# Performance work log

Measured on AMD Instinct MI355X. Metric: run time of the kernel, lower is better.

## Reference

```python
import jax, jax.numpy as jnp
import numpy as np

B, N, C, F, OUT = 4, 512, 1024, 1024, 1024
LOC = 128  # min(128, out_channels)
EPS_BN = 1e-5


def _batchnorm(x, g, b):
    # BatchNorm1d in training mode: biased batch stats over rows
    m = jnp.mean(x, axis=0)
    v = jnp.var(x, axis=0)
    return (x - m) / jnp.sqrt(v + EPS_BN) * g + b


def _relative_pe(loc):
    # loc: [N,4] (x,y,w,h) -> [N,N,LOC]; faithfully replicates the torch
    # cat([N,4N]) -> view(-1,4) interleaving of the original code.
    cx = loc[:, 0] + 0.5 * loc[:, 2]
    cy = loc[:, 1] + 0.5 * loc[:, 3]
    w, h = loc[:, 2], loc[:, 3]
    eps = jnp.float32(1e-3)
    dx = jnp.maximum(jnp.abs(cx[:, None] - cx[None, :]) / w[None, :], eps)
    dy = jnp.maximum(jnp.abs(cy[:, None] - cy[None, :]) / h[None, :], eps)
    dw = w[:, None] / w[None, :]
    dh = h[:, None] / h[None, :]
    delta = jnp.log(jnp.concatenate([dx, dy, dw, dh], axis=-1))  # [N,4N]
    delta = delta.reshape(-1, 4)                                  # [N*N,4]
    d = LOC // 8
    pe = jnp.exp(2.0 * jnp.arange(d, dtype=jnp.float32) / d * np.log(1000.0))
    ang = delta[:, :, None] / pe                                  # [N*N,4,d]
    emb = jnp.concatenate([jnp.sin(ang), jnp.cos(ang)], axis=-1)  # [N*N,4,2d]
    return emb.reshape(N, N, LOC)


def reference(box_features, boxes, bn1_g, bn1_b, Wq, bq, Wk, bk, Wv, bv, Wr, br, bn2_g, bn2_b):
    feat = _batchnorm(box_features, bn1_g, bn1_b).reshape(B, N, C)

    def per_image(f, loc):
        rel = jnp.squeeze(_relative_pe(loc) @ Wr + br, axis=-1)   # [N,N]
        q = f @ Wq + bq
        k = f @ Wk + bk
        v = f @ Wv + bv
        att = q @ k.T / jnp.sqrt(jnp.float32(F)) + jax.nn.log_softmax(rel, axis=-1)
        return jax.nn.softmax(att, axis=-1) @ v                   # [N,OUT]

    out = jax.vmap(per_image)(feat, boxes).reshape(B * N, OUT)
    return _batchnorm(out, bn2_g, bn2_b)


def setup_inputs() -> dict:
    key = jax.random.key(0)
    ks = jax.random.split(key, 10)
    box_features = jax.random.normal(ks[0], (B * N, C), dtype=jnp.float32)
    u = jax.random.uniform(ks[1], (B, N, 4), dtype=jnp.float32)
    xy = u[..., :2] * 800.0
    wh = 16.0 + u[..., 2:] * 240.0
    boxes = jnp.concatenate([xy, wh], axis=-1)
    s = 0.02
    return {
        "box_features": box_features,
        "boxes": boxes,
        "bn1_g": jnp.ones((C,), jnp.float32),
        "bn1_b": jnp.zeros((C,), jnp.float32),
        "Wq": jax.random.normal(ks[2], (C, F), jnp.float32) * s,
        "bq": jnp.zeros((F,), jnp.float32),
        "Wk": jax.random.normal(ks[3], (C, F), jnp.float32) * s,
        "bk": jnp.zeros((F,), jnp.float32),
        "Wv": jax.random.normal(ks[4], (C, OUT), jnp.float32) * s,
        "bv": jnp.zeros((OUT,), jnp.float32),
        "Wr": jax.random.normal(ks[5], (LOC, 1), jnp.float32) * s,
        "br": jnp.zeros((1,), jnp.float32),
        "bn2_g": jnp.ones((OUT,), jnp.float32),
        "bn2_b": jnp.zeros((OUT,), jnp.float32),
    }
```

## Files before the change

kernel.cpp:

```cpp
#include <hip/hip_runtime.h>
#include <math.h>

typedef __bf16 bf16;
typedef __attribute__((ext_vector_type(8))) __bf16 bf16x8;
typedef __attribute__((ext_vector_type(4))) __bf16 bf16x4;
typedef __attribute__((ext_vector_type(4))) float f32x4;

#define NCH1 128
#define RPC1 16

#define XD0   (-6.93f)
#define XSPAN (11.03f)
#define XINVH (1023.f / 11.03f)

__global__ __launch_bounds__(256)
void prep(const float* __restrict__ Wq, const float* __restrict__ Wk, const float* __restrict__ Wv,
          bf16* __restrict__ T0, bf16* __restrict__ T1, bf16* __restrict__ T2,
          const float* __restrict__ bq, const float* __restrict__ bk, float* __restrict__ biasqk,
          const float* __restrict__ X, float* __restrict__ psum, float* __restrict__ psq,
          const float* __restrict__ boxes, const float* __restrict__ Wr, const float* __restrict__ br,
          float* __restrict__ ent, float* __restrict__ tabs)
{
    __shared__ float tile[64][65];
    const int bid = blockIdx.x;
    const int tid = threadIdx.x;

    if (bid < 768) {
        const int mat = bid >> 8, g2 = bid & 255;
        const float* W = (mat == 0) ? Wq : (mat == 1) ? Wk : Wv;
        bf16* T        = (mat == 0) ? T0 : (mat == 1) ? T1 : T2;
        const int bx = (g2 & 15) * 64, by = (g2 >> 4) * 64;
        const int tx = tid & 63, ty = tid >> 6;
#pragma unroll
        for (int i = 0; i < 16; ++i)
            tile[ty + i * 4][tx] = W[(long)(by + ty + i * 4) * 1024 + bx + tx];
        __syncthreads();
#pragma unroll
        for (int i = 0; i < 16; ++i)
            T[(long)(bx + ty + i * 4) * 1024 + by + tx] = (bf16)tile[tx][ty + i * 4];
    } else if (bid < 896) {
        const int c4 = tid;
        const long r0 = (long)(bid - 768) * RPC1;
        const float4* Xv = (const float4*)X;
        float4 s = {0.f,0.f,0.f,0.f}, q = {0.f,0.f,0.f,0.f};
#pragma unroll
        for (int r = 0; r < RPC1; ++r) {
            float4 x = Xv[(r0 + r) * 256 + c4];
            s.x += x.x; s.y += x.y; s.z += x.z; s.w += x.w;
            q.x += x.x*x.x; q.y += x.y*x.y; q.z += x.z*x.z; q.w += x.w*x.w;
        }
        ((float4*)psum)[(bid - 768) * 256 + c4] = s;
        ((float4*)psq) [(bid - 768) * 256 + c4] = q;
    } else if (bid == 896) {
        for (int e = tid; e < 2048; e += 256) {
            float4 b4 = ((const float4*)boxes)[e];
            float w = b4.z, h = b4.w;
            ent[0*2048+e] = b4.x + 0.5f * w;
            ent[1*2048+e] = b4.y + 0.5f * h;
            ent[2*2048+e] = __logf(w);
            ent[3*2048+e] = __logf(h);
            ent[4*2048+e] = 1e-3f * w;
            ent[5*2048+e] = 1e-3f * h;
        }
        for (int i = tid; i < 2048; i += 256)
            biasqk[i] = (i < 1024) ? bq[i] : bk[i - 1024];
    } else {
        const int c = bid - 897;
        float* tb = tabs + c * 1024;
        const float brq = 0.25f * br[0];
        const float hstep = XSPAN / 1023.f;
        for (int e = tid; e < 1024; e += 256) {
            float d = XD0 + hstep * (float)e;
            float a = brq;
#pragma unroll
            for (int k = 0; k < 16; ++k) {
                float tk = exp2f(-1.24572303558f * (float)k);
                float s_, c_;
                __sincosf(d * tk, &s_, &c_);
                a += s_ * Wr[c * 32 + k] + c_ * Wr[c * 32 + 16 + k];
            }
            tb[e] = a;
        }
    }
}

template <int NCH_, int BF16OUT>
__global__ __launch_bounds__(256)
void bn_final_apply(const float* __restrict__ X, const float* __restrict__ psum,
                    const float* __restrict__ psq, const float* __restrict__ g,
                    const float* __restrict__ b, void* __restrict__ Yp)
{
    __shared__ float ls[4][64], lq[4][64], ssc[64], ssh[64];
    const int t  = threadIdx.x;
    const int cs = blockIdx.x;
    const int rc = blockIdx.y;
    const int col_l = t & 63, part = t >> 6;
    const int col = cs * 64 + col_l;
    constexpr int CPT = NCH_ / 4;
    float s = 0.f, q = 0.f;
#pragma unroll
    for (int i = 0; i < CPT; ++i) {
        int ch = part * CPT + i;
        s += psum[ch * 1024 + col];
        q += psq [ch * 1024 + col];
    }
    ls[part][col_l] = s; lq[part][col_l] = q;
    __syncthreads();
    if (t < 64) {
        float S = ls[0][t]+ls[1][t]+ls[2][t]+ls[3][t];
        float Q = lq[0][t]+lq[1][t]+lq[2][t]+lq[3][t];
        float m = S / 2048.f;
        float v = Q / 2048.f - m*m;
        float inv = 1.0f / sqrtf(v + 1e-5f);
        float sc = g[cs*64+t] * inv;
        ssc[t] = sc; ssh[t] = b[cs*64+t] - m*sc;
    }
    __syncthreads();
    const int f = t & 15, rsub = t >> 4;
    float4 sc4 = ((const float4*)ssc)[f];
    float4 sh4 = ((const float4*)ssh)[f];
#pragma unroll
    for (int it = 0; it < 8; ++it) {
        int row = rc*128 + it*16 + rsub;
        float4 x = ((const float4*)(X + (long)row*1024 + cs*64))[f];
        float4 rv;
        rv.x = x.x*sc4.x + sh4.x;
        rv.y = x.y*sc4.y + sh4.y;
        rv.z = x.z*sc4.z + sh4.z;
        rv.w = x.w*sc4.w + sh4.w;
        if constexpr (BF16OUT) {
            bf16x4 y;
            y[0]=(bf16)rv.x; y[1]=(bf16)rv.y; y[2]=(bf16)rv.z; y[3]=(bf16)rv.w;
            ((bf16x4*)((bf16*)Yp + (long)row*1024 + cs*64))[f] = y;
        } else {
            ((float4*)((float*)Yp + (long)row*1024 + cs*64))[f] = rv;
        }
    }
}

__device__ __forceinline__ float look(const float* tab, float d)
{
    float t = (d - XD0) * XINVH;
    t = fminf(fmaxf(t, 0.f), 1022.999f);
    float fi = floorf(t);
    int i = (int)fi;
    float a = tab[i], b = tab[i + 1];
    return a + (b - a) * (t - fi);
}

__device__ __forceinline__ void stage_tile_128x32(const bf16* __restrict__ src_base, int ld,
                                                  int row0, int k0, bf16* lds_base, int w, int l)
{
#pragma unroll
    for (int t = 0; t < 2; ++t) {
        int rchunk = w * 32 + t * 16;
        const bf16* src = src_base + (long)(row0 + rchunk + (l >> 2)) * ld + k0 + (l & 3) * 8;
        __builtin_amdgcn_global_load_lds((__attribute__((address_space(1))) void*)src,
                                         (__attribute__((address_space(3))) void*)(lds_base + rchunk * 32),
                                         16, 0, 0);
    }
}

__device__ __forceinline__ void stage64(const bf16* __restrict__ src_base, int ld,
                                        int row0, int k0, bf16* lds_base, int w, int l)
{
    const bf16* src = src_base + (long)(row0 + w * 16 + (l >> 2)) * ld + k0 + (l & 3) * 8;
    __builtin_amdgcn_global_load_lds((__attribute__((address_space(1))) void*)src,
                                     (__attribute__((address_space(3))) void*)(lds_base + w * 16 * 32),
                                     16, 0, 0);
}

template <int MODE>
__device__ __forceinline__ void gemm_body(
    const bf16* __restrict__ Ab, int lda, const bf16* __restrict__ Bb, int ldb,
    bf16* __restrict__ Cp, int ldc, int K, int bm, int bn,
    const float* __restrict__ bias, char* smem)
{
    bf16* As0 = (bf16*)smem;
    bf16* Bs0 = (bf16*)(smem + 16384);
    const int tid = threadIdx.x;
    const int w = tid >> 6, l = tid & 63;
    const int wr = w >> 1, wc = w & 1;

    f32x4 acc[4][4];
#pragma unroll
    for (int i = 0; i < 4; ++i)
#pragma unroll
        for (int j = 0; j < 4; ++j) acc[i][j] = (f32x4){0.f,0.f,0.f,0.f};

    const int nkt = K >> 5;
    stage_tile_128x32(Ab, lda, bm, 0, As0, w, l);
    stage_tile_128x32(Bb, ldb, bn, 0, Bs0, w, l);
    __syncthreads();

    const int fr = l & 15;
    const int ko = (l >> 4) * 8;

    for (int kt = 0; kt < nkt; ++kt) {
        const int cur = kt & 1;
        bf16* Asc = As0 + cur * 4096;
        bf16* Bsc = Bs0 + cur * 4096;
        if (kt + 1 < nkt) {
            stage_tile_128x32(Ab, lda, bm, (kt + 1) << 5, As0 + (cur ^ 1) * 4096, w, l);
            stage_tile_128x32(Bb, ldb, bn, (kt + 1) << 5, Bs0 + (cur ^ 1) * 4096, w, l);
        }
        bf16x8 af[4], bfv[4];
#pragma unroll
        for (int mi = 0; mi < 4; ++mi)
            af[mi] = *(const bf16x8*)(&Asc[(wr * 64 + mi * 16 + fr) * 32 + ko]);
#pragma unroll
        for (int ni = 0; ni < 4; ++ni)
            bfv[ni] = *(const bf16x8*)(&Bsc[(wc * 64 + ni * 16 + fr) * 32 + ko]);
#pragma unroll
        for (int mi = 0; mi < 4; ++mi)
#pragma unroll
            for (int ni = 0; ni < 4; ++ni)
                acc[mi][ni] = __builtin_amdgcn_mfma_f32_16x16x32_bf16(af[mi], bfv[ni], acc[mi][ni], 0, 0, 0);
        __syncthreads();
    }

    const int crow0 = bm + wr * 64 + (l >> 4) * 4;
    const int ccol0 = bn + wc * 64 + fr;
#pragma unroll
    for (int mi = 0; mi < 4; ++mi)
#pragma unroll
        for (int ni = 0; ni < 4; ++ni)
#pragma unroll
            for (int r = 0; r < 4; ++r) {
                const int row = crow0 + mi * 16 + r;
                const int col = ccol0 + ni * 16;
                const float v = acc[mi][ni][r];
                if constexpr (MODE == 0) {
                    Cp[(long)row * ldc + col] = (bf16)(v + bias[col]);
                } else {
                    Cp[(long)row * ldc + col] = (bf16)(v + bias[row]);
                }
            }
}

__global__ __launch_bounds__(256, 2)
void megaGEMM(const bf16* __restrict__ featbf, const bf16* __restrict__ WqkT,
              const bf16* __restrict__ WvT, bf16* __restrict__ qkbf, bf16* __restrict__ vTbf,
              const float* __restrict__ biasqk, const float* __restrict__ bv)
{
    __shared__ char smem[32768];
    const unsigned bid = (blockIdx.x % 8u) * 48u + (blockIdx.x / 8u);
    const unsigned g = bid / 3u, r = bid % 3u;
    if (r < 2) {
        const unsigned t = g * 2 + r;
        gemm_body<0>(featbf, 1024, WqkT, 1024, qkbf, 2048, 1024,
                     (t & 15) * 128, (t >> 4) * 128, biasqk, smem);
    } else {
        const int img = g >> 5, rem = g & 31;
        gemm_body<1>(WvT, 1024, featbf + (long)img * 524288, 1024,
                     vTbf + (long)img * 524288, 512, 1024,
                     (rem >> 2) * 128, (rem & 3) * 128, bv, smem);
    }
}

__global__ __launch_bounds__(256, 4)
void attn64(const bf16* __restrict__ qk, float* __restrict__ S0, float* __restrict__ S1,
            const float* __restrict__ ent, const float* __restrict__ tabs)
{
    __shared__ char smem[20480];
    const int img = blockIdx.z >> 1, kh = blockIdx.z & 1;
    const int bm = blockIdx.x * 64, bn = blockIdx.y * 64;
    const bf16* A = qk + (long)img * 1048576 + kh * 512;
    const bf16* B = qk + 1024 + (long)img * 1048576 + kh * 512;
    bf16* As0 = (bf16*)smem;
    bf16* Bs0 = (bf16*)(smem + 8192);

    const int tid = threadIdx.x;
    const int w = tid >> 6, l = tid & 63;
    const int wr = w >> 1, wc = w & 1;
    const int fr = l & 15;
    const int ko = (l >> 4) * 8;

    f32x4 acc[2][2];
#pragma unroll
    for (int i = 0; i < 2; ++i)
#pragma unroll
        for (int j = 0; j < 2; ++j) acc[i][j] = (f32x4){0.f,0.f,0.f,0.f};

    stage64(A, 2048, bm, 0, As0, w, l);
    stage64(B, 2048, bn, 0, Bs0, w, l);
    __syncthreads();

    for (int kt = 0; kt < 16; ++kt) {
        const int cur = kt & 1;
        bf16* Asc = As0 + cur * 2048;
        bf16* Bsc = Bs0 + cur * 2048;
        if (kt + 1 < 16) {
            stage64(A, 2048, bm, (kt + 1) << 5, As0 + (cur ^ 1) * 2048, w, l);
            stage64(B, 2048, bn, (kt + 1) << 5, Bs0 + (cur ^ 1) * 2048, w, l);
        }
        bf16x8 af[2], bfv[2];
#pragma unroll
        for (int mi = 0; mi < 2; ++mi)
            af[mi] = *(const bf16x8*)(&Asc[(wr * 32 + mi * 16 + fr) * 32 + ko]);
#pragma unroll
        for (int ni = 0; ni < 2; ++ni)
            bfv[ni] = *(const bf16x8*)(&Bsc[(wc * 32 + ni * 16 + fr) * 32 + ko]);
#pragma unroll
        for (int mi = 0; mi < 2; ++mi)
#pragma unroll
            for (int ni = 0; ni < 2; ++ni)
                acc[mi][ni] = __builtin_amdgcn_mfma_f32_16x16x32_bf16(af[mi], bfv[ni], acc[mi][ni], 0, 0, 0);
        __syncthreads();
    }

    const float scale = 0.03125f;
    float* Sout = (kh == 0 ? S0 : S1) + (long)img * 262144;

    if (kh == 1) {
#pragma unroll
        for (int mi = 0; mi < 2; ++mi)
#pragma unroll
            for (int ni = 0; ni < 2; ++ni)
#pragma unroll
                for (int r = 0; r < 4; ++r) {
                    const int rowl = wr * 32 + mi * 16 + (l >> 4) * 4 + r;
                    const int coll = wc * 32 + ni * 16 + fr;
                    Sout[(long)(bm + rowl) * 512 + bn + coll] = acc[mi][ni][r] * scale;
                }
        return;
    }

    float* stab = (float*)smem;
    float* RA   = stab + 4096;
    float* SA   = RA + 64;
    float* SE   = SA + 260;
    float* SL   = SE + 260;
    const int b   = bn >> 7;
    const int jj0 = (bn & 64) * 4;
    for (int i = tid; i < 4096; i += 256) stab[i] = tabs[i];
    {
        const int eb = img * 512;
        if (tid < 64) RA[tid] = ent[b * 2048 + eb + bm + tid];
        for (int u = tid; u < 260 && jj0 + u < 512; u += 256) {
            SA[u] = ent[b * 2048 + eb + jj0 + u];
            if (b < 2) {
                SE[u] = ent[(4 + b) * 2048 + eb + jj0 + u];
                SL[u] = ent[(2 + b) * 2048 + eb + jj0 + u];
            }
        }
    }
    __syncthreads();
#pragma unroll
    for (int ni = 0; ni < 2; ++ni) {
        const int coll = wc * 32 + ni * 16 + fr;
        const int u0   = 4 * coll;
        const float sA0 = SA[u0], sA1 = SA[u0+1], sA2 = SA[u0+2], sA3 = SA[u0+3];
        float sE0=0.f,sE1=0.f,sE2=0.f,sE3=0.f, sL0=0.f,sL1=0.f,sL2=0.f,sL3=0.f;
        if (b < 2) {
            sE0 = SE[u0]; sE1 = SE[u0+1]; sE2 = SE[u0+2]; sE3 = SE[u0+3];
            sL0 = SL[u0]; sL1 = SL[u0+1]; sL2 = SL[u0+2]; sL3 = SL[u0+3];
        }
#pragma unroll
        for (int mi = 0; mi < 2; ++mi)
#pragma unroll
            for (int r = 0; r < 4; ++r) {
                const int rowl = wr * 32 + mi * 16 + (l >> 4) * 4 + r;
                const float ai = RA[rowl];
                float d0, d1, d2, d3;
                if (b < 2) {
                    d0 = __logf(fmaxf(fabsf(ai - sA0), sE0)) - sL0;
                    d1 = __logf(fmaxf(fabsf(ai - sA1), sE1)) - sL1;
                    d2 = __logf(fmaxf(fabsf(ai - sA2), sE2)) - sL2;
                    d3 = __logf(fmaxf(fabsf(ai - sA3), sE3)) - sL3;
                } else {
                    d0 = ai - sA0; d1 = ai - sA1; d2 = ai - sA2; d3 = ai - sA3;
                }
                float relv = look(stab,        d0) + look(stab + 1024, d1)
                           + look(stab + 2048, d2) + look(stab + 3072, d3);
                Sout[(long)(bm + rowl) * 512 + bn + coll] = acc[mi][ni][r] * scale + relv;
            }
    }
}

__global__ __launch_bounds__(256)
void softmax2(const float* __restrict__ S0, const float* __restrict__ S1, bf16* __restrict__ P)
{
    const long row = blockIdx.x;
    const int t = threadIdx.x;
    float x0 = S0[row * 512 + t]       + S1[row * 512 + t];
    float x1 = S0[row * 512 + t + 256] + S1[row * 512 + t + 256];
    float mx = fmaxf(x0, x1);
#pragma unroll
    for (int off = 32; off; off >>= 1) mx = fmaxf(mx, __shfl_xor(mx, off));
    __shared__ float redm[4], reds[4];
    if ((t & 63) == 0) redm[t >> 6] = mx;
    __syncthreads();
    mx = fmaxf(fmaxf(redm[0], redm[1]), fmaxf(redm[2], redm[3]));
    float e0 = __expf(x0 - mx), e1 = __expf(x1 - mx);
    float sm = e0 + e1;
#pragma unroll
    for (int off = 32; off; off >>= 1) sm += __shfl_xor(sm, off);
    if ((t & 63) == 0) reds[t >> 6] = sm;
    __syncthreads();
    sm = (reds[0] + reds[1]) + (reds[2] + reds[3]);
    float inv = 1.0f / sm;
    P[row * 512 + t]       = (bf16)(e0 * inv);
    P[row * 512 + t + 256] = (bf16)(e1 * inv);
}

__global__ __launch_bounds__(256, 4)
void pv64(const bf16* __restrict__ P, const bf16* __restrict__ vT, float* __restrict__ out,
          float* __restrict__ psum, float* __restrict__ psq)
{
    __shared__ char smem[16384];
    const int img = blockIdx.z;
    const int bm = blockIdx.x * 64, bn = blockIdx.y * 64;
    const bf16* A = P  + (long)img * 262144;
    const bf16* B = vT + (long)img * 524288;
    float* C = out + (long)img * 524288;
    bf16* As0 = (bf16*)smem;
    bf16* Bs0 = (bf16*)(smem + 8192);

    const int tid = threadIdx.x;
    const int w = tid >> 6, l = tid & 63;
    const int wr = w >> 1, wc = w & 1;
    const int fr = l & 15;
    const int ko = (l >> 4) * 8;

    f32x4 acc[2][2];
#pragma unroll
    for (int i = 0; i < 2; ++i)
#pragma unroll
        for (int j = 0; j < 2; ++j) acc[i][j] = (f32x4){0.f,0.f,0.f,0.f};

    stage64(A, 512, bm, 0, As0, w, l);
    stage64(B, 512, bn, 0, Bs0, w, l);
    __syncthreads();

    for (int kt = 0; kt < 16; ++kt) {
        const int cur = kt & 1;
        bf16* Asc = As0 + cur * 2048;
        bf16* Bsc = Bs0 + cur * 2048;
        if (kt + 1 < 16) {
            stage64(A, 512, bm, (kt + 1) << 5, As0 + (cur ^ 1) * 2048, w, l);
            stage64(B, 512, bn, (kt + 1) << 5, Bs0 + (cur ^ 1) * 2048, w, l);
        }
        bf16x8 af[2], bfv[2];
#pragma unroll
        for (int mi = 0; mi < 2; ++mi)
            af[mi] = *(const bf16x8*)(&Asc[(wr * 32 + mi * 16 + fr) * 32 + ko]);
#pragma unroll
        for (int ni = 0; ni < 2; ++ni)
            bfv[ni] = *(const bf16x8*)(&Bsc[(wc * 32 + ni * 16 + fr) * 32 + ko]);
#pragma unroll
        for (int mi = 0; mi < 2; ++mi)
#pragma unroll
            for (int ni = 0; ni < 2; ++ni)
                acc[mi][ni] = __builtin_amdgcn_mfma_f32_16x16x32_bf16(af[mi], bfv[ni], acc[mi][ni], 0, 0, 0);
        __syncthreads();
    }

#pragma unroll
    for (int mi = 0; mi < 2; ++mi)
#pragma unroll
        for (int ni = 0; ni < 2; ++ni)
#pragma unroll
            for (int r = 0; r < 4; ++r) {
                const int rowl = wr * 32 + mi * 16 + (l >> 4) * 4 + r;
                const int coll = wc * 32 + ni * 16 + fr;
                C[(long)(bm + rowl) * 1024 + bn + coll] = acc[mi][ni][r];
            }

    float s_[2], q_[2];
#pragma unroll
    for (int ni = 0; ni < 2; ++ni) {
        float s = 0.f, q = 0.f;
#pragma unroll
        for (int mi = 0; mi < 2; ++mi)
#pragma unroll
            for (int r = 0; r < 4; ++r) { float v = acc[mi][ni][r]; s += v; q += v * v; }
        s_[ni] = s; q_[ni] = q;
    }
#pragma unroll
    for (int ni = 0; ni < 2; ++ni) {
        s_[ni] += __shfl_xor(s_[ni], 16); s_[ni] += __shfl_xor(s_[ni], 32);
        q_[ni] += __shfl_xor(q_[ni], 16); q_[ni] += __shfl_xor(q_[ni], 32);
    }
    float* lred = (float*)smem;
    __syncthreads();
    if (l < 16) {
#pragma unroll
        for (int ni = 0; ni < 2; ++ni) {
            const int c = wc * 32 + ni * 16 + l;
            lred[(wr * 2 + 0) * 64 + c] = s_[ni];
            lred[(wr * 2 + 1) * 64 + c] = q_[ni];
        }
    }
    __syncthreads();
    if (tid < 64) {
        const int chunk = img * 8 + blockIdx.x;
        psum[chunk * 1024 + bn + tid] = lred[0 * 64 + tid] + lred[2 * 64 + tid];
        psq [chunk * 1024 + bn + tid] = lred[1 * 64 + tid] + lred[3 * 64 + tid];
    }
}

extern "C" void kernel_launch(void* const* d_in, const int* in_sizes, int n_in,
                              void* d_out, int out_size, void* d_ws, size_t ws_size,
                              hipStream_t stream)
{
    const float* box_features = (const float*)d_in[0];
    const float* boxes  = (const float*)d_in[1];
    const float* bn1_g  = (const float*)d_in[2];
    const float* bn1_b  = (const float*)d_in[3];
    const float* Wq     = (const float*)d_in[4];
    const float* bq     = (const float*)d_in[5];
    const float* Wk     = (const float*)d_in[6];
    const float* bk     = (const float*)d_in[7];
    const float* Wv     = (const float*)d_in[8];
    const float* bv     = (const float*)d_in[9];
    const float* Wr     = (const float*)d_in[10];
    const float* br     = (const float*)d_in[11];
    const float* bn2_g  = (const float*)d_in[12];
    const float* bn2_b  = (const float*)d_in[13];
    float* out = (float*)d_out;

    char* ws = (char*)d_ws;
    const long MB = 1024 * 1024;
    float* psum   = (float*)(ws + 0);
    float* psq    = (float*)(ws + 512 * 1024);
    float* biasqk = (float*)(ws + 1 * MB);
    float* ent    = (float*)(ws + 1 * MB + 65536);
    float* tabs   = (float*)(ws + 1 * MB + 131072);
    bf16*  featbf = (bf16*)(ws + 2 * MB);
    bf16*  WqkT   = (bf16*)(ws + 6 * MB);
    float* Sbuf1  = (float*)(ws + 6 * MB);
    bf16*  WvT    = (bf16*)(ws + 10 * MB);
    bf16*  qkbf   = (bf16*)(ws + 12 * MB);
    bf16*  vTbf   = (bf16*)(ws + 20 * MB);
    float* Sbuf0  = (float*)(ws + 24 * MB);
    bf16*  Pbuf   = (bf16*)(ws + 28 * MB);

    prep<<<dim3(901, 1, 1), dim3(256, 1, 1), 0, stream>>>(
        Wq, Wk, Wv, WqkT, WqkT + 1024 * 1024, WvT, bq, bk, biasqk,
        box_features, psum, psq, boxes, Wr, br, ent, tabs);

    bn_final_apply<NCH1, 1><<<dim3(16, 16, 1), dim3(256, 1, 1), 0, stream>>>(
        box_features, psum, psq, bn1_g, bn1_b, featbf);

    megaGEMM<<<dim3(384, 1, 1), dim3(256, 1, 1), 0, stream>>>(
        featbf, WqkT, WvT, qkbf, vTbf, biasqk, bv);

    attn64<<<dim3(8, 8, 8), dim3(256, 1, 1), 0, stream>>>(qkbf, Sbuf0, Sbuf1, ent, tabs);

    softmax2<<<dim3(2048, 1, 1), dim3(256, 1, 1), 0, stream>>>(Sbuf0, Sbuf1, Pbuf);

    pv64<<<dim3(8, 16, 4), dim3(256, 1, 1), 0, stream>>>(Pbuf, vTbf, out, psum, psq);

    bn_final_apply<32, 0><<<dim3(16, 16, 1), dim3(256, 1, 1), 0, stream>>>(
        out, psum, psq, bn2_g, bn2_b, out);
}
```

Baseline: 86.82 us.

## Deepen GEMM K-tile to 64 with XOR-swizzled LDS layout

The projection GEMM now stages 128x64 K-tiles instead of 128x32, halving the number of barrier-separated iterations, and stores rows in LDS with an XOR swizzle of the 16-byte groups so fragment reads avoid bank conflicts. LDS use grows from 32KB to 64KB per block. That may lower how many blocks fit per CU, which is relevant because launch bounds request 2 blocks.

```diff
diff --git a/kernel.cpp b/kernel.cpp
--- a/kernel.cpp
+++ b/kernel.cpp
@@ -148,17 +148,25 @@
     return a + (b - a) * (t - fi);
 }
 
-__device__ __forceinline__ void stage_tile_128x32(const bf16* __restrict__ src_base, int ld,
-                                                  int row0, int k0, bf16* lds_base, int w, int l)
-{
-#pragma unroll
-    for (int t = 0; t < 2; ++t) {
-        int rchunk = w * 32 + t * 16;
-        const bf16* src = src_base + (long)(row0 + rchunk + (l >> 2)) * ld + k0 + (l & 3) * 8;
+__device__ __forceinline__ void stage_128x64_swz(const bf16* __restrict__ src_base, int ld,
+                                                 int row0, int k0, bf16* lds_base, int w, int l)
+{
+    const int rsub = l >> 3;
+    const int gsrc = ((l & 7) ^ rsub) * 8;
+#pragma unroll
+    for (int t = 0; t < 4; ++t) {
+        const int rchunk = w * 32 + t * 8;
+        const bf16* src = src_base + (long)(row0 + rchunk + rsub) * ld + k0 + gsrc;
         __builtin_amdgcn_global_load_lds((__attribute__((address_space(1))) void*)src,
-                                         (__attribute__((address_space(3))) void*)(lds_base + rchunk * 32),
+                                         (__attribute__((address_space(3))) void*)(lds_base + rchunk * 64),
                                          16, 0, 0);
     }
+}
+
+__device__ __forceinline__ bf16x8 frag_swz(const bf16* __restrict__ Ts, int row, int kk, int lo)
+{
+    const int gp = ((kk << 2) + lo) ^ (row & 7);
+    return *(const bf16x8*)(Ts + row * 64 + gp * 8);
 }
 
 __device__ __forceinline__ void stage64(const bf16* __restrict__ src_base, int ld,
@@ -177,7 +185,7 @@
     const float* __restrict__ bias, char* smem)
 {
     bf16* As0 = (bf16*)smem;
-    bf16* Bs0 = (bf16*)(smem + 16384);
+    bf16* Bs0 = (bf16*)(smem + 32768);
     const int tid = threadIdx.x;
     const int w = tid >> 6, l = tid & 63;
     const int wr = w >> 1, wc = w & 1;
@@ -188,38 +196,41 @@
 #pragma unroll
         for (int j = 0; j < 4; ++j) acc[i][j] = (f32x4){0.f,0.f,0.f,0.f};
 
-    const int nkt = K >> 5;
-    stage_tile_128x32(Ab, lda, bm, 0, As0, w, l);
-    stage_tile_128x32(Bb, ldb, bn, 0, Bs0, w, l);
+    const int nkt = K >> 6;
+    stage_128x64_swz(Ab, lda, bm, 0, As0, w, l);
+    stage_128x64_swz(Bb, ldb, bn, 0, Bs0, w, l);
     __syncthreads();
 
     const int fr = l & 15;
-    const int ko = (l >> 4) * 8;
+    const int lo = l >> 4;
 
     for (int kt = 0; kt < nkt; ++kt) {
         const int cur = kt & 1;
-        bf16* Asc = As0 + cur * 4096;
-        bf16* Bsc = Bs0 + cur * 4096;
+        bf16* Asc = As0 + cur * 8192;
+        bf16* Bsc = Bs0 + cur * 8192;
         if (kt + 1 < nkt) {
-            stage_tile_128x32(Ab, lda, bm, (kt + 1) << 5, As0 + (cur ^ 1) * 4096, w, l);
-            stage_tile_128x32(Bb, ldb, bn, (kt + 1) << 5, Bs0 + (cur ^ 1) * 4096, w, l);
-        }
-        bf16x8 af[4], bfv[4];
-#pragma unroll
-        for (int mi = 0; mi < 4; ++mi)
-            af[mi] = *(const bf16x8*)(&Asc[(wr * 64 + mi * 16 + fr) * 32 + ko]);
-#pragma unroll
-        for (int ni = 0; ni < 4; ++ni)
-            bfv[ni] = *(const bf16x8*)(&Bsc[(wc * 64 + ni * 16 + fr) * 32 + ko]);
-#pragma unroll
-        for (int mi = 0; mi < 4; ++mi)
+            stage_128x64_swz(Ab, lda, bm, (kt + 1) << 6, As0 + (cur ^ 1) * 8192, w, l);
+            stage_128x64_swz(Bb, ldb, bn, (kt + 1) << 6, Bs0 + (cur ^ 1) * 8192, w, l);
+        }
+#pragma unroll
+        for (int kk = 0; kk < 2; ++kk) {
+            bf16x8 af[4], bfv[4];
+#pragma unroll
+            for (int mi = 0; mi < 4; ++mi)
+                af[mi] = frag_swz(Asc, wr * 64 + mi * 16 + fr, kk, lo);
 #pragma unroll
             for (int ni = 0; ni < 4; ++ni)
-                acc[mi][ni] = __builtin_amdgcn_mfma_f32_16x16x32_bf16(af[mi], bfv[ni], acc[mi][ni], 0, 0, 0);
+                bfv[ni] = frag_swz(Bsc, wc * 64 + ni * 16 + fr, kk, lo);
+#pragma unroll
+            for (int mi = 0; mi < 4; ++mi)
+#pragma unroll
+                for (int ni = 0; ni < 4; ++ni)
+                    acc[mi][ni] = __builtin_amdgcn_mfma_f32_16x16x32_bf16(af[mi], bfv[ni], acc[mi][ni], 0, 0, 0);
+        }
         __syncthreads();
     }
 
-    const int crow0 = bm + wr * 64 + (l >> 4) * 4;
+    const int crow0 = bm + wr * 64 + lo * 4;
     const int ccol0 = bn + wc * 64 + fr;
 #pragma unroll
     for (int mi = 0; mi < 4; ++mi)
@@ -243,7 +254,7 @@
               const bf16* __restrict__ WvT, bf16* __restrict__ qkbf, bf16* __restrict__ vTbf,
               const float* __restrict__ biasqk, const float* __restrict__ bv)
 {
-    __shared__ char smem[32768];
+    __shared__ char smem[65536];
     const unsigned bid = (blockIdx.x % 8u) * 48u + (blockIdx.x / 8u);
     const unsigned g = bid / 3u, r = bid % 3u;
     if (r < 2) {
```

New measurement: 82.45 us. 5.0% less time.
